# Kernel tuning notes

Measured on AMD Instinct MI355X. Metric: run time of the kernel, lower is better.

Reference implementation:

```python
import jax, jax.numpy as jnp
import numpy as np

B, P, N, E, IN, HID, NL, MULT = 4, 8, 2000, 2000, 16, 128, 3, 4
LOGIT_CLIP = 10.0

def setup_inputs() -> dict:
    key = jax.random.key(0)
    ks = jax.random.split(key, 8)
    s = 0.05
    return {
        "node_features": jax.random.normal(ks[0], (B, P, N, IN), jnp.float32),
        "incidence": jax.random.uniform(ks[1], (B, N, E), jnp.float32),  # weighted incidence
        "W_in": s * jax.random.normal(ks[2], (IN, HID), jnp.float32),
        "edge_Ws": s * jax.random.normal(ks[3], (NL, HID, HID), jnp.float32),
        "node_Ws": s * jax.random.normal(ks[4], (NL, HID, HID), jnp.float32),
        "W1": s * jax.random.normal(ks[5], (HID, MULT * HID), jnp.float32),
        "W2": s * jax.random.normal(ks[6], (MULT * HID, HID), jnp.float32),
        "W_dec": s * jax.random.normal(ks[7], (HID, 1), jnp.float32),
    }

def reference(node_features, incidence, W_in, edge_Ws, node_Ws, W1, W2, W_dec):
    # node_features: [B,P,N,in]; incidence H: [B,N,E] (broadcast over P instead of torch's repeat)
    x = node_features @ W_in                                   # [B,P,N,h]
    H = incidence
    n_layers = edge_Ws.shape[0]
    for l in range(n_layers):
        # node -> hyperedge aggregation: H^T @ x
        e = jnp.einsum('bne,bpnd->bped', H, x)                 # [B,P,E,h]
        e = jax.nn.relu(e @ edge_Ws[l])
        # hyperedge -> node aggregation: H @ e
        x = jnp.einsum('bne,bped->bpnd', H, e)                 # [B,P,N,h]
        x = jax.nn.relu(x @ node_Ws[l])
    # MLP: Linear -> ReLU -> Linear (dropout = 0)
    h = jax.nn.relu(x @ W1) @ W2                               # [B,P,N,h]
    out = h @ W_dec                                            # [B,P,N,1]
    out = out / jnp.sqrt(jnp.asarray(W_in.shape[1], jnp.float32))
    out = LOGIT_CLIP * jnp.tanh(out)
    return out
```

## Files before the change

kernel.cpp:

```cpp
#include <hip/hip_runtime.h>
#include <hip/hip_bf16.h>


typedef __attribute__((ext_vector_type(8))) short bf16x8;
typedef __attribute__((ext_vector_type(4))) float f32x4;

#define GLL16(gp, lp) __builtin_amdgcn_global_load_lds(                      \
    (const __attribute__((address_space(1))) void*)(gp),                     \
    (__attribute__((address_space(3))) void*)(lp), 16, 0, 0)

__device__ __forceinline__ unsigned short f2bf(float v) {
  __hip_bfloat16 h = __float2bfloat16(v);
  return __builtin_bit_cast(unsigned short, h);
}
__device__ __forceinline__ float bf2f(unsigned short u) {
  unsigned int x = ((unsigned int)u) << 16;
  return __builtin_bit_cast(float, x);
}

__global__ void convH_k(const float* __restrict__ H,
                        unsigned short* __restrict__ Hb,
                        unsigned short* __restrict__ HTb) {
  int b  = blockIdx.z;
  int n0 = blockIdx.y * 32, e0 = blockIdx.x * 32;
  __shared__ float t[32][33];
  int tx = threadIdx.x & 31, ty = threadIdx.x >> 5;
  for (int r = ty; r < 32; r += 8) {
    int n = n0 + r, e = e0 + tx;
    float v = (n < 2000 && e < 2000) ? H[((long)b * 2000 + n) * 2000 + e] : 0.f;
    t[r][tx] = v;
    Hb[((long)b * 2048 + n) * 2048 + e] = f2bf(v);
  }
  __syncthreads();
  for (int r = ty; r < 32; r += 8) {
    HTb[((long)b * 2048 + (e0 + r)) * 2048 + (n0 + tx)] = f2bf(t[tx][r]);
  }
}

__global__ void transposeW_k(const float* __restrict__ src,
                             unsigned short* __restrict__ dst, int R, int C) {
  __shared__ float t[32][33];
  int c0 = blockIdx.x * 32, r0 = blockIdx.y * 32;
  int tx = threadIdx.x & 31, ty = threadIdx.x >> 5;
  for (int rr = ty; rr < 32; rr += 8) {
    int rI = r0 + rr, cI = c0 + tx;
    t[rr][tx] = (rI < R && cI < C) ? src[(long)rI * C + cI] : 0.f;
  }
  __syncthreads();
  for (int rr = ty; rr < 32; rr += 8) {
    int cO = c0 + rr, rO = r0 + tx;
    if (cO < C && rO < R) dst[(long)cO * R + rO] = f2bf(t[tx][rr]);
  }
}

__global__ __launch_bounds__(256) void x0_k(
    const float* __restrict__ nf, const float* __restrict__ Win,
    unsigned short* __restrict__ xb, unsigned short* __restrict__ xTb) {
  __shared__ float nfs[128][16];
  __shared__ float wins[2048];
  __shared__ unsigned short xt[128][136];

  int bp = blockIdx.y;
  int n0 = blockIdx.x * 128;
  int tid = threadIdx.x;

  {
    int r = tid >> 1, c = (tid & 1) * 8;
    int n = n0 + r;
    float4 v0 = make_float4(0.f, 0.f, 0.f, 0.f), v1 = v0;
    if (n < 2000) {
      const float* src = nf + ((long)bp * 2000 + n) * 16 + c;
      v0 = *(const float4*)src;
      v1 = *(const float4*)(src + 4);
    }
    *(float4*)&nfs[r][c]     = v0;
    *(float4*)&nfs[r][c + 4] = v1;
  }
  {
    int base = tid * 8;
    float4 a = *(const float4*)(Win + base);
    float4 b = *(const float4*)(Win + base + 4);
    *(float4*)&wins[base]     = a;
    *(float4*)&wins[base + 4] = b;
  }
  __syncthreads();

  int d = tid & 127, half = tid >> 7;
  float wcol[16];
#pragma unroll
  for (int k = 0; k < 16; k++) wcol[k] = wins[k * 128 + d];

  unsigned short* xtRow = xTb + ((long)bp * 128 + d) * 2048 + n0 + half * 64;
#pragma unroll
  for (int oct = 0; oct < 8; oct++) {
    bf16x8 pk;
#pragma unroll
    for (int j = 0; j < 8; j++) {
      int nl = half * 64 + oct * 8 + j;
      float v = 0.f;
#pragma unroll
      for (int k = 0; k < 16; k++) v += nfs[nl][k] * wcol[k];
      unsigned short bits = f2bf(v);
      pk[j] = (short)bits;
      xt[nl][d] = bits;
    }
    *(bf16x8*)(xtRow + oct * 8) = pk;
  }
  __syncthreads();

  {
    int r = tid >> 1, c0 = (tid & 1) * 64;
    unsigned short* dst = xb + ((long)bp * 2048 + n0 + r) * 128 + c0;
#pragma unroll
    for (int i = 0; i < 8; i++) {
      bf16x8 v = *(const bf16x8*)&xt[r][c0 + i * 8];
      *(bf16x8*)(dst + i * 8) = v;
    }
  }
}

__global__ void wfuse_k(const float* __restrict__ W2, const float* __restrict__ Wdec,
                        float* __restrict__ wf) {
  int i = blockIdx.x * 256 + threadIdx.x;
  if (i < 512) {
    float s = 0.f;
#pragma unroll 8
    for (int j = 0; j < 128; j++) s += W2[i * 128 + j] * Wdec[j];
    wf[i] = s;
  }
}

template <int WN, int WT>
__global__ __launch_bounds__(256, 2) void gemm_fused(
    const unsigned short* __restrict__ A, int lda, long strideA, int aDiv,
    const unsigned short* __restrict__ BT, int ldbt, long strideBT,
    const unsigned short* __restrict__ Wt,
    unsigned short* __restrict__ Cn, int ldc, long strideCn,
    unsigned short* __restrict__ Ct, int ldct, long strideCt, int K) {
  int wgid = blockIdx.x;
  int orig = (wgid & 7) * 64 + (wgid >> 3);
  int mblk = orig & 15;
  int bz   = orig >> 4;
  A  += (long)(bz / aDiv) * strideA;
  BT += (long)bz * strideBT;
  int m0 = mblk * 128;

  __shared__ unsigned short smem[32768];

  int tid  = threadIdx.x;
  int lane = tid & 63;
  int w    = tid >> 6;
  int wr   = w >> 1, wc = w & 1;
  int fr   = lane & 15;
  int fg   = lane >> 4;

  int srow   = tid >> 3;
  int schunk = ((tid & 7) ^ (srow & 7)) * 8;
  const unsigned short* Agp[4];
  const unsigned short* Bgp[4];
#pragma unroll
  for (int i = 0; i < 4; i++) {
    Agp[i] = A + (long)(m0 + i * 32 + srow) * lda + schunk;
    Bgp[i] = BT + (long)(i * 32 + srow) * ldbt + schunk;
  }

#define STAGE(sel, tk) do {                                                  \
    long _k = (long)(tk) * 64;                                               \
    _Pragma("unroll")                                                        \
    for (int i = 0; i < 4; i++)                                              \
      GLL16(Agp[i] + _k, smem + (sel) * 16384 + (i * 256 + tid) * 8);        \
    _Pragma("unroll")                                                        \
    for (int i = 0; i < 4; i++)                                              \
      GLL16(Bgp[i] + _k, smem + (sel) * 16384 + 8192 + (i * 256 + tid) * 8); \
  } while (0)

  f32x4 acc[4][4] = {};
  const int cOff0 = (fg ^ (fr & 7)) * 8;
  const int cOff1 = ((4 + fg) ^ (fr & 7)) * 8;

#define PHASE(Asp, Bsp, CO) do {                                             \
    bf16x8 af[4], bv[4];                                                     \
    _Pragma("unroll")                                                        \
    for (int m = 0; m < 4; m++)                                              \
      af[m] = *(const bf16x8*)&(Asp)[(wr * 64 + m * 16 + fr) * 64 + (CO)];   \
    _Pragma("unroll")                                                        \
    for (int n = 0; n < 4; n++)                                              \
      bv[n] = *(const bf16x8*)&(Bsp)[(wc * 64 + n * 16 + fr) * 64 + (CO)];   \
    __builtin_amdgcn_s_setprio(1);                                           \
    _Pragma("unroll")                                                        \
    for (int m = 0; m < 4; m++)                                              \
      _Pragma("unroll")                                                      \
      for (int n = 0; n < 4; n++)                                            \
        acc[m][n] = __builtin_amdgcn_mfma_f32_16x16x32_bf16(af[m], bv[n],    \
                                                            acc[m][n], 0, 0, 0); \
    __builtin_amdgcn_s_setprio(0);                                           \
  } while (0)

#define COMPUTE64(sel) do {                                                  \
    const unsigned short* As_ = smem + (sel) * 16384;                        \
    const unsigned short* Bs_ = As_ + 8192;                                  \
    PHASE(As_, Bs_, cOff0);                                                  \
    PHASE(As_, Bs_, cOff1);                                                  \
  } while (0)

#define VMW(n) asm volatile("s_waitcnt vmcnt(" #n ")" ::: "memory")
#define BARR __builtin_amdgcn_s_barrier()
#define SCH0 __builtin_amdgcn_sched_barrier(0)

  int nt2 = K >> 6;

  STAGE(0, 0);
  int t = 0;
  for (; t + 2 < nt2; t += 2) {
    STAGE(1, t + 1);
    VMW(8); BARR; SCH0;
    COMPUTE64(0);
    BARR;
    STAGE(0, t + 2);
    VMW(8); BARR; SCH0;
    COMPUTE64(1);
    BARR;
  }
  STAGE(1, nt2 - 1);
  VMW(8); BARR; SCH0;
  COMPUTE64(0);
  BARR;
  VMW(0); BARR; SCH0;
  COMPUTE64(1);
#undef STAGE
#undef COMPUTE64
#undef PHASE

  unsigned short* Gs = smem;
#pragma unroll
  for (int m = 0; m < 4; m++) {
#pragma unroll
    for (int n = 0; n < 4; n++) {
      int rowb = wr * 64 + m * 16 + fg * 4;
      int col  = wc * 64 + n * 16 + fr;
      int ch = col >> 3, ci = col & 7;
#pragma unroll
      for (int r = 0; r < 4; r++) {
        int row = rowb + r;
        Gs[row * 128 + ((ch ^ (row & 7)) * 8) + ci] = f2bf(acc[m][n][r]);
      }
    }
  }
  __syncthreads();

  f32x4 acc2[4][4] = {};
#pragma unroll
  for (int kk = 0; kk < 4; kk++) {
    bf16x8 a2[4], b2[4];
#pragma unroll
    for (int m = 0; m < 4; m++) {
      int row = wr * 64 + m * 16 + fr;
      int c = kk * 4 + fg;
      a2[m] = *(const bf16x8*)&Gs[row * 128 + ((c ^ (fr & 7)) * 8)];
    }
#pragma unroll
    for (int n = 0; n < 4; n++) {
      int row = wc * 64 + n * 16 + fr;
      b2[n] = *(const bf16x8*)&Wt[row * 128 + (kk * 4 + fg) * 8];
    }
#pragma unroll
    for (int m = 0; m < 4; m++)
#pragma unroll
      for (int n = 0; n < 4; n++)
        acc2[m][n] = __builtin_amdgcn_mfma_f32_16x16x32_bf16(a2[m], b2[n], acc2[m][n], 0, 0, 0);
  }

  if (WN) {
#pragma unroll
    for (int m = 0; m < 4; m++) {
#pragma unroll
      for (int n = 0; n < 4; n++) {
        int rowb = m0 + wr * 64 + m * 16 + fg * 4;
        int col  = wc * 64 + n * 16 + fr;
        unsigned short* p = Cn + bz * strideCn + (long)rowb * ldc + col;
        p[0]       = f2bf(fmaxf(acc2[m][n][0], 0.f));
        p[ldc]     = f2bf(fmaxf(acc2[m][n][1], 0.f));
        p[2 * ldc] = f2bf(fmaxf(acc2[m][n][2], 0.f));
        p[3 * ldc] = f2bf(fmaxf(acc2[m][n][3], 0.f));
      }
    }
  }

  if (WT) {
    __syncthreads();
    unsigned short* GsT = smem;
#pragma unroll
    for (int m = 0; m < 4; m++) {
#pragma unroll
      for (int n = 0; n < 4; n++) {
        int rowb = wr * 64 + m * 16 + fg * 4;
        int col  = wc * 64 + n * 16 + fr;
        int chunk = rowb >> 3;
        ushort4 pk;
        pk.x = f2bf(fmaxf(acc2[m][n][0], 0.f));
        pk.y = f2bf(fmaxf(acc2[m][n][1], 0.f));
        pk.z = f2bf(fmaxf(acc2[m][n][2], 0.f));
        pk.w = f2bf(fmaxf(acc2[m][n][3], 0.f));
        *(ushort4*)&GsT[col * 128 + ((chunk ^ (col & 7)) * 8) + (rowb & 7)] = pk;
      }
    }
    __syncthreads();
    unsigned short* CtB = Ct + bz * strideCt + m0;
#pragma unroll
    for (int i = 0; i < 8; i++) {
      int s = i * 256 + tid;
      int col = s >> 4, slot = s & 15;
      int l = slot ^ (col & 7);
      bf16x8 v = *(const bf16x8*)&GsT[col * 128 + slot * 8];
      *(bf16x8*)(CtB + (long)col * ldct + l * 8) = v;
    }
  }
}

__global__ __launch_bounds__(256) void mlp_k(
    const unsigned short* __restrict__ X,
    const unsigned short* __restrict__ W1T,
    const float* __restrict__ wf,
    float* __restrict__ out) {
  __shared__ unsigned short Xs[128 * 128];
  __shared__ unsigned short Bs[128 * 128];
  __shared__ float rowacc[128];

  int tid  = threadIdx.x;
  int lane = tid & 63;
  int w    = tid >> 6, wr = w >> 1, wc = w & 1;
  int fr   = lane & 15, fg = lane >> 4;
  long m0  = (long)blockIdx.x * 128;

#pragma unroll
  for (int i = 0; i < 8; i++) {
    int s = i * 256 + tid;
    int r = s >> 4, c = (s & 15) ^ (r & 7);
    GLL16(X + (m0 + r) * 128 + c * 8, (unsigned short*)Xs + s * 8);
  }
  if (tid < 128) rowacc[tid] = 0.f;

  float rs[4][4] = {};

  for (int nb = 0; nb < 4; nb++) {
#pragma unroll
    for (int i = 0; i < 8; i++) {
      int s = i * 256 + tid;
      int r = s >> 4, c = (s & 15) ^ (r & 7);
      GLL16(W1T + (long)(nb * 128 + r) * 128 + c * 8, (unsigned short*)Bs + s * 8);
    }
    __syncthreads();

    f32x4 acc[4][4] = {};
#pragma unroll
    for (int kk = 0; kk < 4; kk++) {
      bf16x8 a2[4], b2[4];
#pragma unroll
      for (int m = 0; m < 4; m++) {
        int row = wr * 64 + m * 16 + fr;
        int c = kk * 4 + fg;
        a2[m] = *(const bf16x8*)&Xs[row * 128 + ((c ^ (row & 7)) * 8)];
      }
#pragma unroll
      for (int n = 0; n < 4; n++) {
        int row = wc * 64 + n * 16 + fr;
        int c = kk * 4 + fg;
        b2[n] = *(const bf16x8*)&Bs[row * 128 + ((c ^ (row & 7)) * 8)];
      }
#pragma unroll
      for (int m = 0; m < 4; m++)
#pragma unroll
        for (int n = 0; n < 4; n++)
          acc[m][n] = __builtin_amdgcn_mfma_f32_16x16x32_bf16(a2[m], b2[n], acc[m][n], 0, 0, 0);
    }

#pragma unroll
    for (int n = 0; n < 4; n++) {
      float wv = wf[nb * 128 + wc * 64 + n * 16 + fr];
#pragma unroll
      for (int m = 0; m < 4; m++)
#pragma unroll
        for (int r = 0; r < 4; r++)
          rs[m][r] += fmaxf(acc[m][n][r], 0.f) * wv;
    }
    __syncthreads();
  }

#pragma unroll
  for (int m = 0; m < 4; m++)
#pragma unroll
    for (int r = 0; r < 4; r++) {
      float v = rs[m][r];
      v += __shfl_xor(v, 1, 64);
      v += __shfl_xor(v, 2, 64);
      v += __shfl_xor(v, 4, 64);
      v += __shfl_xor(v, 8, 64);
      if (fr == 0) atomicAdd(&rowacc[wr * 64 + m * 16 + fg * 4 + r], v);
    }
  __syncthreads();

  if (tid < 128) {
    long row = m0 + tid;
    int bp = (int)(row >> 11), n = (int)(row & 2047);
    if (n < 2000)
      out[(long)bp * 2000 + n] = 10.f * tanhf(rowacc[tid] * 0.08838834764831843f);
  }
}

extern "C" void kernel_launch(void* const* d_in, const int* in_sizes, int n_in,
                              void* d_out, int out_size, void* d_ws, size_t ws_size,
                              hipStream_t stream) {
  const float* nf    = (const float*)d_in[0];
  const float* H     = (const float*)d_in[1];
  const float* Win   = (const float*)d_in[2];
  const float* edgeW = (const float*)d_in[3];
  const float* nodeW = (const float*)d_in[4];
  const float* W1    = (const float*)d_in[5];
  const float* W2    = (const float*)d_in[6];
  const float* Wdec  = (const float*)d_in[7];
  float* out = (float*)d_out;

  char* ws = (char*)d_ws;
  unsigned short* Hb   = (unsigned short*)(ws + 0);
  unsigned short* HTb  = (unsigned short*)(ws + 33554432);
  unsigned short* xb   = (unsigned short*)(ws + 67108864);
  unsigned short* xTb  = (unsigned short*)(ws + 83886080);
  unsigned short* eTb  = (unsigned short*)(ws + 100663296);
  unsigned short* edgeWT = (unsigned short*)(ws + 117440512);
  unsigned short* nodeWT = (unsigned short*)(ws + 117538816);
  unsigned short* W1T    = (unsigned short*)(ws + 117637120);
  float*          wf     = (float*)(ws + 117768192);
  (void)ws_size; (void)in_sizes; (void)n_in; (void)out_size;

  convH_k<<<dim3(64, 64, 4), 256, 0, stream>>>(H, Hb, HTb);
  for (int l = 0; l < 3; l++) {
    transposeW_k<<<dim3(4, 4), 256, 0, stream>>>(edgeW + l * 16384, edgeWT + l * 16384, 128, 128);
    transposeW_k<<<dim3(4, 4), 256, 0, stream>>>(nodeW + l * 16384, nodeWT + l * 16384, 128, 128);
  }
  transposeW_k<<<dim3(16, 4), 256, 0, stream>>>(W1, W1T, 128, 512);
  wfuse_k<<<2, 256, 0, stream>>>(W2, Wdec, wf);
  x0_k<<<dim3(16, 32), 256, 0, stream>>>(nf, Win, xb, xTb);

  for (int l = 0; l < 3; l++) {
    gemm_fused<0, 1><<<dim3(512), 256, 0, stream>>>(
        HTb, 2048, 2048L * 2048, 8, xTb, 2048, 128L * 2048,
        edgeWT + l * 16384,
        nullptr, 0, 0, eTb, 2048, 128L * 2048, 2048);
    if (l < 2) {
      gemm_fused<0, 1><<<dim3(512), 256, 0, stream>>>(
          Hb, 2048, 2048L * 2048, 8, eTb, 2048, 128L * 2048,
          nodeWT + l * 16384,
          nullptr, 0, 0, xTb, 2048, 128L * 2048, 2048);
    } else {
      gemm_fused<1, 1><<<dim3(512), 256, 0, stream>>>(
          Hb, 2048, 2048L * 2048, 8, eTb, 2048, 128L * 2048,
          nodeWT + l * 16384,
          xb, 128, 2048L * 128, xTb, 2048, 128L * 2048, 2048);
    }
  }

  mlp_k<<<dim3(512), 256, 0, stream>>>(xb, W1T, wf, out);
}
```

Baseline: 313.8 us.

## Replace LDS double-buffered staging with direct global loads into MFMA fragments

Removes the global_load_lds double-buffered pipeline with its barriers and swizzled LDS tiles. Each wave now loads its A and B fragments straight from global memory into registers every K-step. LDS shrinks to a single 128x128 epilogue buffer, which may raise occupancy. In exchange, reuse of the tile across waves through LDS is lost, so each wave re-reads data from global/L2, and loads are no longer overlapped with compute by an explicit prefetch.

```diff
diff --git a/kernel.cpp b/kernel.cpp
--- a/kernel.cpp
+++ b/kernel.cpp
@@ -145,7 +145,7 @@
   BT += (long)bz * strideBT;
   int m0 = mblk * 128;
 
-  __shared__ unsigned short smem[32768];
+  __shared__ unsigned short Gs[128 * 128];
 
   int tid  = threadIdx.x;
   int lane = tid & 63;
@@ -154,84 +154,41 @@
   int fr   = lane & 15;
   int fg   = lane >> 4;
 
-  int srow   = tid >> 3;
-  int schunk = ((tid & 7) ^ (srow & 7)) * 8;
-  const unsigned short* Agp[4];
-  const unsigned short* Bgp[4];
-#pragma unroll
-  for (int i = 0; i < 4; i++) {
-    Agp[i] = A + (long)(m0 + i * 32 + srow) * lda + schunk;
-    Bgp[i] = BT + (long)(i * 32 + srow) * ldbt + schunk;
-  }
-
-#define STAGE(sel, tk) do {                                                  \
-    long _k = (long)(tk) * 64;                                               \
-    _Pragma("unroll")                                                        \
-    for (int i = 0; i < 4; i++)                                              \
-      GLL16(Agp[i] + _k, smem + (sel) * 16384 + (i * 256 + tid) * 8);        \
-    _Pragma("unroll")                                                        \
-    for (int i = 0; i < 4; i++)                                              \
-      GLL16(Bgp[i] + _k, smem + (sel) * 16384 + 8192 + (i * 256 + tid) * 8); \
-  } while (0)
+  const unsigned short* Arow[4];
+  const unsigned short* Bcol[4];
+#pragma unroll
+  for (int m = 0; m < 4; m++)
+    Arow[m] = A + (long)(m0 + wr * 64 + m * 16 + fr) * lda + fg * 8;
+#pragma unroll
+  for (int n = 0; n < 4; n++)
+    Bcol[n] = BT + (long)(wc * 64 + n * 16 + fr) * ldbt + fg * 8;
 
   f32x4 acc[4][4] = {};
-  const int cOff0 = (fg ^ (fr & 7)) * 8;
-  const int cOff1 = ((4 + fg) ^ (fr & 7)) * 8;
-
-#define PHASE(Asp, Bsp, CO) do {                                             \
-    bf16x8 af[4], bv[4];                                                     \
-    _Pragma("unroll")                                                        \
-    for (int m = 0; m < 4; m++)                                              \
-      af[m] = *(const bf16x8*)&(Asp)[(wr * 64 + m * 16 + fr) * 64 + (CO)];   \
-    _Pragma("unroll")                                                        \
-    for (int n = 0; n < 4; n++)                                              \
-      bv[n] = *(const bf16x8*)&(Bsp)[(wc * 64 + n * 16 + fr) * 64 + (CO)];   \
-    __builtin_amdgcn_s_setprio(1);                                           \
-    _Pragma("unroll")                                                        \
-    for (int m = 0; m < 4; m++)                                              \
-      _Pragma("unroll")                                                      \
-      for (int n = 0; n < 4; n++)                                            \
-        acc[m][n] = __builtin_amdgcn_mfma_f32_16x16x32_bf16(af[m], bv[n],    \
-                                                            acc[m][n], 0, 0, 0); \
-    __builtin_amdgcn_s_setprio(0);                                           \
-  } while (0)
-
-#define COMPUTE64(sel) do {                                                  \
-    const unsigned short* As_ = smem + (sel) * 16384;                        \
-    const unsigned short* Bs_ = As_ + 8192;                                  \
-    PHASE(As_, Bs_, cOff0);                                                  \
-    PHASE(As_, Bs_, cOff1);                                                  \
-  } while (0)
-
-#define VMW(n) asm volatile("s_waitcnt vmcnt(" #n ")" ::: "memory")
-#define BARR __builtin_amdgcn_s_barrier()
-#define SCH0 __builtin_amdgcn_sched_barrier(0)
-
-  int nt2 = K >> 6;
-
-  STAGE(0, 0);
-  int t = 0;
-  for (; t + 2 < nt2; t += 2) {
-    STAGE(1, t + 1);
-    VMW(8); BARR; SCH0;
-    COMPUTE64(0);
-    BARR;
-    STAGE(0, t + 2);
-    VMW(8); BARR; SCH0;
-    COMPUTE64(1);
-    BARR;
-  }
-  STAGE(1, nt2 - 1);
-  VMW(8); BARR; SCH0;
-  COMPUTE64(0);
-  BARR;
-  VMW(0); BARR; SCH0;
-  COMPUTE64(1);
-#undef STAGE
-#undef COMPUTE64
-#undef PHASE
-
-  unsigned short* Gs = smem;
+
+  for (int k0 = 0; k0 < K; k0 += 64) {
+    bf16x8 a0[4], a1[4], b0[4], b1[4];
+#pragma unroll
+    for (int m = 0; m < 4; m++) {
+      a0[m] = *(const bf16x8*)(Arow[m] + k0);
+      a1[m] = *(const bf16x8*)(Arow[m] + k0 + 32);
+    }
+#pragma unroll
+    for (int n = 0; n < 4; n++) {
+      b0[n] = *(const bf16x8*)(Bcol[n] + k0);
+      b1[n] = *(const bf16x8*)(Bcol[n] + k0 + 32);
+    }
+#pragma unroll
+    for (int m = 0; m < 4; m++)
+#pragma unroll
+      for (int n = 0; n < 4; n++)
+        acc[m][n] = __builtin_amdgcn_mfma_f32_16x16x32_bf16(a0[m], b0[n], acc[m][n], 0, 0, 0);
+#pragma unroll
+    for (int m = 0; m < 4; m++)
+#pragma unroll
+      for (int n = 0; n < 4; n++)
+        acc[m][n] = __builtin_amdgcn_mfma_f32_16x16x32_bf16(a1[m], b1[n], acc[m][n], 0, 0, 0);
+  }
+
 #pragma unroll
   for (int m = 0; m < 4; m++) {
 #pragma unroll
@@ -288,7 +245,7 @@
 
   if (WT) {
     __syncthreads();
-    unsigned short* GsT = smem;
+    unsigned short* GsT = Gs;
 #pragma unroll
     for (int m = 0; m < 4; m++) {
 #pragma unroll
```

After: 816.0 us. 160% more time.

## Split K across two wave groups per block with LDS reduction in fused GEMM

Applied to the files above, without the earlier changes.

The fused hypergraph GEMM now launches 512 threads per block, split into two 256-thread groups. Each group handles half of the K dimension with its own double-buffered 32-wide K tiles in shared memory. The partial accumulators are then summed through an fp32 LDS reduction before group 0 runs the weight GEMM and the epilogue. The aim is more waves per CU to hide memory latency on a grid of only 512 blocks. In exchange it adds an LDS reduction with extra barriers, leaves half the threads idle in the epilogue, and increases register pressure under the stricter launch bounds.

```diff
diff --git a/kernel.cpp b/kernel.cpp
--- a/kernel.cpp
+++ b/kernel.cpp
@@ -131,7 +131,7 @@
 }
 
 template <int WN, int WT>
-__global__ __launch_bounds__(256, 2) void gemm_fused(
+__global__ __launch_bounds__(512, 4) void gemm_fused(
     const unsigned short* __restrict__ A, int lda, long strideA, int aDiv,
     const unsigned short* __restrict__ BT, int ldbt, long strideBT,
     const unsigned short* __restrict__ Wt,
@@ -148,44 +148,47 @@
   __shared__ unsigned short smem[32768];
 
   int tid  = threadIdx.x;
+  int grp  = tid >> 8;
+  int gtid = tid & 255;
   int lane = tid & 63;
-  int w    = tid >> 6;
-  int wr   = w >> 1, wc = w & 1;
+  int wig  = (tid >> 6) & 3;
+  int wr   = wig >> 1, wc = wig & 1;
   int fr   = lane & 15;
   int fg   = lane >> 4;
 
-  int srow   = tid >> 3;
-  int schunk = ((tid & 7) ^ (srow & 7)) * 8;
-  const unsigned short* Agp[4];
-  const unsigned short* Bgp[4];
-#pragma unroll
-  for (int i = 0; i < 4; i++) {
-    Agp[i] = A + (long)(m0 + i * 32 + srow) * lda + schunk;
-    Bgp[i] = BT + (long)(i * 32 + srow) * ldbt + schunk;
-  }
+  int kbase = grp * (K >> 1);
+  int nt = (K >> 1) >> 5;
+
+  int ch0 = gtid, ch1 = gtid + 256;
+  int r0_ = ch0 >> 2, gc0 = (ch0 & 3) ^ ((r0_ >> 1) & 3);
+  int r1_ = ch1 >> 2, gc1 = (ch1 & 3) ^ ((r1_ >> 1) & 3);
+  const unsigned short* Ag0 = A + (long)(m0 + r0_) * lda + kbase + gc0 * 8;
+  const unsigned short* Ag1 = A + (long)(m0 + r1_) * lda + kbase + gc1 * 8;
+  const unsigned short* Bg0 = BT + (long)r0_ * ldbt + kbase + gc0 * 8;
+  const unsigned short* Bg1 = BT + (long)r1_ * ldbt + kbase + gc1 * 8;
+  unsigned short* db = smem + grp * 16384;
 
 #define STAGE(sel, tk) do {                                                  \
-    long _k = (long)(tk) * 64;                                               \
-    _Pragma("unroll")                                                        \
-    for (int i = 0; i < 4; i++)                                              \
-      GLL16(Agp[i] + _k, smem + (sel) * 16384 + (i * 256 + tid) * 8);        \
-    _Pragma("unroll")                                                        \
-    for (int i = 0; i < 4; i++)                                              \
-      GLL16(Bgp[i] + _k, smem + (sel) * 16384 + 8192 + (i * 256 + tid) * 8); \
+    int _k = (tk) * 32;                                                      \
+    GLL16(Ag0 + _k, db + (sel) * 8192 + ch0 * 8);                            \
+    GLL16(Ag1 + _k, db + (sel) * 8192 + ch1 * 8);                            \
+    GLL16(Bg0 + _k, db + (sel) * 8192 + 4096 + ch0 * 8);                     \
+    GLL16(Bg1 + _k, db + (sel) * 8192 + 4096 + ch1 * 8);                     \
   } while (0)
 
   f32x4 acc[4][4] = {};
-  const int cOff0 = (fg ^ (fr & 7)) * 8;
-  const int cOff1 = ((4 + fg) ^ (fr & 7)) * 8;
-
-#define PHASE(Asp, Bsp, CO) do {                                             \
+  const int cIdx = (fg ^ ((fr >> 1) & 3)) * 8;
+
+#define COMPUTE(sel) do {                                                    \
+    const unsigned short* As_ = db + (sel) * 8192;                           \
+    const unsigned short* Bs_ = As_ + 4096;                                  \
     bf16x8 af[4], bv[4];                                                     \
     _Pragma("unroll")                                                        \
     for (int m = 0; m < 4; m++)                                              \
-      af[m] = *(const bf16x8*)&(Asp)[(wr * 64 + m * 16 + fr) * 64 + (CO)];   \
+      af[m] = *(const bf16x8*)&As_[(wr * 64 + m * 16 + fr) * 32 + cIdx];     \
     _Pragma("unroll")                                                        \
     for (int n = 0; n < 4; n++)                                              \
-      bv[n] = *(const bf16x8*)&(Bsp)[(wc * 64 + n * 16 + fr) * 64 + (CO)];   \
+      bv[n] = *(const bf16x8*)&Bs_[(wc * 64 + n * 16 + fr) * 32 + cIdx];     \
     __builtin_amdgcn_s_setprio(1);                                           \
     _Pragma("unroll")                                                        \
     for (int m = 0; m < 4; m++)                                              \
@@ -196,92 +199,113 @@
     __builtin_amdgcn_s_setprio(0);                                           \
   } while (0)
 
-#define COMPUTE64(sel) do {                                                  \
-    const unsigned short* As_ = smem + (sel) * 16384;                        \
-    const unsigned short* Bs_ = As_ + 8192;                                  \
-    PHASE(As_, Bs_, cOff0);                                                  \
-    PHASE(As_, Bs_, cOff1);                                                  \
-  } while (0)
-
 #define VMW(n) asm volatile("s_waitcnt vmcnt(" #n ")" ::: "memory")
 #define BARR __builtin_amdgcn_s_barrier()
 #define SCH0 __builtin_amdgcn_sched_barrier(0)
 
-  int nt2 = K >> 6;
-
   STAGE(0, 0);
   int t = 0;
-  for (; t + 2 < nt2; t += 2) {
+  for (; t + 2 < nt; t += 2) {
     STAGE(1, t + 1);
-    VMW(8); BARR; SCH0;
-    COMPUTE64(0);
+    VMW(4); BARR; SCH0;
+    COMPUTE(0);
     BARR;
     STAGE(0, t + 2);
-    VMW(8); BARR; SCH0;
-    COMPUTE64(1);
+    VMW(4); BARR; SCH0;
+    COMPUTE(1);
     BARR;
   }
-  STAGE(1, nt2 - 1);
-  VMW(8); BARR; SCH0;
-  COMPUTE64(0);
+  STAGE(1, nt - 1);
+  VMW(4); BARR; SCH0;
+  COMPUTE(0);
   BARR;
   VMW(0); BARR; SCH0;
-  COMPUTE64(1);
+  COMPUTE(1);
 #undef STAGE
-#undef COMPUTE64
-#undef PHASE
+#undef COMPUTE
+
+  float* Lf = (float*)smem;
+  __syncthreads();
+  if (grp == 1) {
+#pragma unroll
+    for (int m = 0; m < 4; m++)
+#pragma unroll
+      for (int n = 0; n < 4; n++) {
+        int rowb = wr * 64 + m * 16 + fg * 4;
+        int col  = wc * 64 + n * 16 + fr;
+#pragma unroll
+        for (int r = 0; r < 4; r++) Lf[(rowb + r) * 128 + col] = acc[m][n][r];
+      }
+  }
+  __syncthreads();
+  if (grp == 0) {
+#pragma unroll
+    for (int m = 0; m < 4; m++)
+#pragma unroll
+      for (int n = 0; n < 4; n++) {
+        int rowb = wr * 64 + m * 16 + fg * 4;
+        int col  = wc * 64 + n * 16 + fr;
+#pragma unroll
+        for (int r = 0; r < 4; r++) acc[m][n][r] += Lf[(rowb + r) * 128 + col];
+      }
+  }
+  __syncthreads();
 
   unsigned short* Gs = smem;
-#pragma unroll
-  for (int m = 0; m < 4; m++) {
-#pragma unroll
-    for (int n = 0; n < 4; n++) {
-      int rowb = wr * 64 + m * 16 + fg * 4;
-      int col  = wc * 64 + n * 16 + fr;
-      int ch = col >> 3, ci = col & 7;
-#pragma unroll
-      for (int r = 0; r < 4; r++) {
-        int row = rowb + r;
-        Gs[row * 128 + ((ch ^ (row & 7)) * 8) + ci] = f2bf(acc[m][n][r]);
+  if (grp == 0) {
+#pragma unroll
+    for (int m = 0; m < 4; m++) {
+#pragma unroll
+      for (int n = 0; n < 4; n++) {
+        int rowb = wr * 64 + m * 16 + fg * 4;
+        int col  = wc * 64 + n * 16 + fr;
+        int ch = col >> 3, ci = col & 7;
+#pragma unroll
+        for (int r = 0; r < 4; r++) {
+          int row = rowb + r;
+          Gs[row * 128 + ((ch ^ (row & 7)) * 8) + ci] = f2bf(acc[m][n][r]);
+        }
       }
     }
   }
   __syncthreads();
 
   f32x4 acc2[4][4] = {};
-#pragma unroll
-  for (int kk = 0; kk < 4; kk++) {
-    bf16x8 a2[4], b2[4];
-#pragma unroll
-    for (int m = 0; m < 4; m++) {
-      int row = wr * 64 + m * 16 + fr;
-      int c = kk * 4 + fg;
-      a2[m] = *(const bf16x8*)&Gs[row * 128 + ((c ^ (fr & 7)) * 8)];
-    }
-#pragma unroll
-    for (int n = 0; n < 4; n++) {
-      int row = wc * 64 + n * 16 + fr;
-      b2[n] = *(const bf16x8*)&Wt[row * 128 + (kk * 4 + fg) * 8];
-    }
-#pragma unroll
-    for (int m = 0; m < 4; m++)
-#pragma unroll
-      for (int n = 0; n < 4; n++)
-        acc2[m][n] = __builtin_amdgcn_mfma_f32_16x16x32_bf16(a2[m], b2[n], acc2[m][n], 0, 0, 0);
-  }
-
-  if (WN) {
-#pragma unroll
-    for (int m = 0; m < 4; m++) {
+  if (grp == 0) {
+#pragma unroll
+    for (int kk = 0; kk < 4; kk++) {
+      bf16x8 a2[4], b2[4];
+#pragma unroll
+      for (int m = 0; m < 4; m++) {
+        int row = wr * 64 + m * 16 + fr;
+        int c = kk * 4 + fg;
+        a2[m] = *(const bf16x8*)&Gs[row * 128 + ((c ^ (fr & 7)) * 8)];
+      }
 #pragma unroll
       for (int n = 0; n < 4; n++) {
-        int rowb = m0 + wr * 64 + m * 16 + fg * 4;
-        int col  = wc * 64 + n * 16 + fr;
-        unsigned short* p = Cn + bz * strideCn + (long)rowb * ldc + col;
-        p[0]       = f2bf(fmaxf(acc2[m][n][0], 0.f));
-        p[ldc]     = f2bf(fmaxf(acc2[m][n][1], 0.f));
-        p[2 * ldc] = f2bf(fmaxf(acc2[m][n][2], 0.f));
-        p[3 * ldc] = f2bf(fmaxf(acc2[m][n][3], 0.f));
+        int row = wc * 64 + n * 16 + fr;
+        b2[n] = *(const bf16x8*)&Wt[row * 128 + (kk * 4 + fg) * 8];
+      }
+#pragma unroll
+      for (int m = 0; m < 4; m++)
+#pragma unroll
+        for (int n = 0; n < 4; n++)
+          acc2[m][n] = __builtin_amdgcn_mfma_f32_16x16x32_bf16(a2[m], b2[n], acc2[m][n], 0, 0, 0);
+    }
+
+    if (WN) {
+#pragma unroll
+      for (int m = 0; m < 4; m++) {
+#pragma unroll
+        for (int n = 0; n < 4; n++) {
+          int rowb = m0 + wr * 64 + m * 16 + fg * 4;
+          int col  = wc * 64 + n * 16 + fr;
+          unsigned short* p = Cn + bz * strideCn + (long)rowb * ldc + col;
+          p[0]       = f2bf(fmaxf(acc2[m][n][0], 0.f));
+          p[ldc]     = f2bf(fmaxf(acc2[m][n][1], 0.f));
+          p[2 * ldc] = f2bf(fmaxf(acc2[m][n][2], 0.f));
+          p[3 * ldc] = f2bf(fmaxf(acc2[m][n][3], 0.f));
+        }
       }
     }
   }
@@ -289,30 +313,34 @@
   if (WT) {
     __syncthreads();
     unsigned short* GsT = smem;
-#pragma unroll
-    for (int m = 0; m < 4; m++) {
-#pragma unroll
-      for (int n = 0; n < 4; n++) {
-        int rowb = wr * 64 + m * 16 + fg * 4;
-        int col  = wc * 64 + n * 16 + fr;
-        int chunk = rowb >> 3;
-        ushort4 pk;
-        pk.x = f2bf(fmaxf(acc2[m][n][0], 0.f));
-        pk.y = f2bf(fmaxf(acc2[m][n][1], 0.f));
-        pk.z = f2bf(fmaxf(acc2[m][n][2], 0.f));
-        pk.w = f2bf(fmaxf(acc2[m][n][3], 0.f));
-        *(ushort4*)&GsT[col * 128 + ((chunk ^ (col & 7)) * 8) + (rowb & 7)] = pk;
+    if (grp == 0) {
+#pragma unroll
+      for (int m = 0; m < 4; m++) {
+#pragma unroll
+        for (int n = 0; n < 4; n++) {
+          int rowb = wr * 64 + m * 16 + fg * 4;
+          int col  = wc * 64 + n * 16 + fr;
+          int chunk = rowb >> 3;
+          ushort4 pk;
+          pk.x = f2bf(fmaxf(acc2[m][n][0], 0.f));
+          pk.y = f2bf(fmaxf(acc2[m][n][1], 0.f));
+          pk.z = f2bf(fmaxf(acc2[m][n][2], 0.f));
+          pk.w = f2bf(fmaxf(acc2[m][n][3], 0.f));
+          *(ushort4*)&GsT[col * 128 + ((chunk ^ (col & 7)) * 8) + (rowb & 7)] = pk;
+        }
       }
     }
     __syncthreads();
-    unsigned short* CtB = Ct + bz * strideCt + m0;
-#pragma unroll
-    for (int i = 0; i < 8; i++) {
-      int s = i * 256 + tid;
-      int col = s >> 4, slot = s & 15;
-      int l = slot ^ (col & 7);
-      bf16x8 v = *(const bf16x8*)&GsT[col * 128 + slot * 8];
-      *(bf16x8*)(CtB + (long)col * ldct + l * 8) = v;
+    if (grp == 0) {
+      unsigned short* CtB = Ct + bz * strideCt + m0;
+#pragma unroll
+      for (int i = 0; i < 8; i++) {
+        int s = i * 256 + gtid;
+        int col = s >> 4, slot = s & 15;
+        int l = slot ^ (col & 7);
+        bf16x8 v = *(const bf16x8*)&GsT[col * 128 + slot * 8];
+        *(bf16x8*)(CtB + (long)col * ldct + l * 8) = v;
+      }
     }
   }
 }
@@ -442,17 +470,17 @@
   x0_k<<<dim3(16, 32), 256, 0, stream>>>(nf, Win, xb, xTb);
 
   for (int l = 0; l < 3; l++) {
-    gemm_fused<0, 1><<<dim3(512), 256, 0, stream>>>(
+    gemm_fused<0, 1><<<dim3(512), 512, 0, stream>>>(
         HTb, 2048, 2048L * 2048, 8, xTb, 2048, 128L * 2048,
         edgeWT + l * 16384,
         nullptr, 0, 0, eTb, 2048, 128L * 2048, 2048);
     if (l < 2) {
-      gemm_fused<0, 1><<<dim3(512), 256, 0, stream>>>(
+      gemm_fused<0, 1><<<dim3(512), 512, 0, stream>>>(
           Hb, 2048, 2048L * 2048, 8, eTb, 2048, 128L * 2048,
           nodeWT + l * 16384,
           nullptr, 0, 0, xTb, 2048, 128L * 2048, 2048);
     } else {
-      gemm_fused<1, 1><<<dim3(512), 256, 0, stream>>>(
+      gemm_fused<1, 1><<<dim3(512), 512, 0, stream>>>(
           Hb, 2048, 2048L * 2048, 8, eTb, 2048, 128L * 2048,
           nodeWT + l * 16384,
           xb, 128, 2048L * 128, xTb, 2048, 128L * 2048, 2048);
```

Result: slower. 379.2 us (+20.8%).

## Enlarge GEMM tile to 256 rows with 8 waves and 4-stage K pipeline

Applied to the files above, without the earlier changes.

The fused hypergraph GEMM now uses 512-thread blocks that each cover 256 output rows, half as many blocks as before. The K-step shrinks to 32, and shared memory becomes a 4-deep ring buffer. Global-to-LDS loads for future stages are issued inside the compute body, after the fragment reads. The aim is better reuse of the B tile across more rows and more overlap of memory latency with MFMA work. In exchange there are more barriers per K, larger LDS use, one block per CU, and a changed transposed-output write pattern.

```diff
diff --git a/kernel.cpp b/kernel.cpp
--- a/kernel.cpp
+++ b/kernel.cpp
@@ -131,61 +131,57 @@
 }
 
 template <int WN, int WT>
-__global__ __launch_bounds__(256, 2) void gemm_fused(
+__global__ __launch_bounds__(512, 1) void gemm_fused(
     const unsigned short* __restrict__ A, int lda, long strideA, int aDiv,
     const unsigned short* __restrict__ BT, int ldbt, long strideBT,
     const unsigned short* __restrict__ Wt,
     unsigned short* __restrict__ Cn, int ldc, long strideCn,
     unsigned short* __restrict__ Ct, int ldct, long strideCt, int K) {
   int wgid = blockIdx.x;
-  int orig = (wgid & 7) * 64 + (wgid >> 3);
-  int mblk = orig & 15;
-  int bz   = orig >> 4;
+  int orig = (wgid & 7) * 32 + (wgid >> 3);
+  int mblk = orig & 7;
+  int bz   = orig >> 3;
   A  += (long)(bz / aDiv) * strideA;
   BT += (long)bz * strideBT;
-  int m0 = mblk * 128;
-
-  __shared__ unsigned short smem[32768];
+  int m0 = mblk * 256;
+
+  __shared__ unsigned short smem[49152];
 
   int tid  = threadIdx.x;
   int lane = tid & 63;
   int w    = tid >> 6;
-  int wr   = w >> 1, wc = w & 1;
+  int wr   = w >> 1;
+  int wc   = w & 1;
   int fr   = lane & 15;
   int fg   = lane >> 4;
 
-  int srow   = tid >> 3;
-  int schunk = ((tid & 7) ^ (srow & 7)) * 8;
-  const unsigned short* Agp[4];
-  const unsigned short* Bgp[4];
-#pragma unroll
-  for (int i = 0; i < 4; i++) {
-    Agp[i] = A + (long)(m0 + i * 32 + srow) * lda + schunk;
-    Bgp[i] = BT + (long)(i * 32 + srow) * ldbt + schunk;
-  }
+  int srow = tid >> 2;
+  int sch  = ((tid & 3) ^ ((srow >> 1) & 3)) * 8;
+  const unsigned short* Ag0 = A + (long)(m0 + srow) * lda + sch;
+  const unsigned short* Ag1 = A + (long)(m0 + 128 + srow) * lda + sch;
+  const unsigned short* Bg  = BT + (long)srow * ldbt + sch;
 
 #define STAGE(sel, tk) do {                                                  \
-    long _k = (long)(tk) * 64;                                               \
-    _Pragma("unroll")                                                        \
-    for (int i = 0; i < 4; i++)                                              \
-      GLL16(Agp[i] + _k, smem + (sel) * 16384 + (i * 256 + tid) * 8);        \
-    _Pragma("unroll")                                                        \
-    for (int i = 0; i < 4; i++)                                              \
-      GLL16(Bgp[i] + _k, smem + (sel) * 16384 + 8192 + (i * 256 + tid) * 8); \
+    int _k = (tk) * 32;                                                      \
+    GLL16(Ag0 + _k, smem + (sel) * 12288 + tid * 8);                         \
+    GLL16(Ag1 + _k, smem + (sel) * 12288 + 4096 + tid * 8);                  \
+    GLL16(Bg + _k,  smem + (sel) * 12288 + 8192 + tid * 8);                  \
   } while (0)
 
   f32x4 acc[4][4] = {};
-  const int cOff0 = (fg ^ (fr & 7)) * 8;
-  const int cOff1 = ((4 + fg) ^ (fr & 7)) * 8;
-
-#define PHASE(Asp, Bsp, CO) do {                                             \
+  const int cIdx = (fg ^ ((fr >> 1) & 3)) * 8;
+
+#define TILEBODY(sel, kst, DO) do {                                          \
+    const unsigned short* As_ = smem + (sel) * 12288;                        \
+    const unsigned short* Bs_ = As_ + 8192;                                  \
     bf16x8 af[4], bv[4];                                                     \
     _Pragma("unroll")                                                        \
     for (int m = 0; m < 4; m++)                                              \
-      af[m] = *(const bf16x8*)&(Asp)[(wr * 64 + m * 16 + fr) * 64 + (CO)];   \
+      af[m] = *(const bf16x8*)&As_[(wr * 64 + m * 16 + fr) * 32 + cIdx];     \
     _Pragma("unroll")                                                        \
     for (int n = 0; n < 4; n++)                                              \
-      bv[n] = *(const bf16x8*)&(Bsp)[(wc * 64 + n * 16 + fr) * 64 + (CO)];   \
+      bv[n] = *(const bf16x8*)&Bs_[(wc * 64 + n * 16 + fr) * 32 + cIdx];     \
+    if (DO) STAGE(((sel) + 3) & 3, kst);                                     \
     __builtin_amdgcn_s_setprio(1);                                           \
     _Pragma("unroll")                                                        \
     for (int m = 0; m < 4; m++)                                              \
@@ -196,40 +192,29 @@
     __builtin_amdgcn_s_setprio(0);                                           \
   } while (0)
 
-#define COMPUTE64(sel) do {                                                  \
-    const unsigned short* As_ = smem + (sel) * 16384;                        \
-    const unsigned short* Bs_ = As_ + 8192;                                  \
-    PHASE(As_, Bs_, cOff0);                                                  \
-    PHASE(As_, Bs_, cOff1);                                                  \
-  } while (0)
-
 #define VMW(n) asm volatile("s_waitcnt vmcnt(" #n ")" ::: "memory")
 #define BARR __builtin_amdgcn_s_barrier()
 #define SCH0 __builtin_amdgcn_sched_barrier(0)
 
-  int nt2 = K >> 6;
+  int nt = K >> 5;
 
   STAGE(0, 0);
-  int t = 0;
-  for (; t + 2 < nt2; t += 2) {
-    STAGE(1, t + 1);
-    VMW(8); BARR; SCH0;
-    COMPUTE64(0);
-    BARR;
-    STAGE(0, t + 2);
-    VMW(8); BARR; SCH0;
-    COMPUTE64(1);
-    BARR;
-  }
-  STAGE(1, nt2 - 1);
-  VMW(8); BARR; SCH0;
-  COMPUTE64(0);
-  BARR;
-  VMW(0); BARR; SCH0;
-  COMPUTE64(1);
+  STAGE(1, 1);
+  STAGE(2, 2);
+  int k = 0;
+  for (; k < nt - 4; k += 4) {
+    VMW(6); BARR; SCH0; TILEBODY(0, k + 3, 1);
+    VMW(6); BARR; SCH0; TILEBODY(1, k + 4, 1);
+    VMW(6); BARR; SCH0; TILEBODY(2, k + 5, 1);
+    VMW(6); BARR; SCH0; TILEBODY(3, k + 6, 1);
+  }
+  VMW(6); BARR; SCH0; TILEBODY(0, nt - 1, 1);
+  VMW(6); BARR; SCH0; TILEBODY(1, 0, 0);
+  VMW(3); BARR; SCH0; TILEBODY(2, 0, 0);
+  VMW(0); BARR; SCH0; TILEBODY(3, 0, 0);
 #undef STAGE
-#undef COMPUTE64
-#undef PHASE
+#undef TILEBODY
+  __syncthreads();
 
   unsigned short* Gs = smem;
 #pragma unroll
@@ -295,24 +280,24 @@
       for (int n = 0; n < 4; n++) {
         int rowb = wr * 64 + m * 16 + fg * 4;
         int col  = wc * 64 + n * 16 + fr;
-        int chunk = rowb >> 3;
+        int slot = (rowb >> 3) ^ (col & 7);
         ushort4 pk;
         pk.x = f2bf(fmaxf(acc2[m][n][0], 0.f));
         pk.y = f2bf(fmaxf(acc2[m][n][1], 0.f));
         pk.z = f2bf(fmaxf(acc2[m][n][2], 0.f));
         pk.w = f2bf(fmaxf(acc2[m][n][3], 0.f));
-        *(ushort4*)&GsT[col * 128 + ((chunk ^ (col & 7)) * 8) + (rowb & 7)] = pk;
+        *(ushort4*)&GsT[col * 256 + slot * 8 + (rowb & 7)] = pk;
       }
     }
     __syncthreads();
     unsigned short* CtB = Ct + bz * strideCt + m0;
-#pragma unroll
-    for (int i = 0; i < 8; i++) {
-      int s = i * 256 + tid;
-      int col = s >> 4, slot = s & 15;
-      int l = slot ^ (col & 7);
-      bf16x8 v = *(const bf16x8*)&GsT[col * 128 + slot * 8];
-      *(bf16x8*)(CtB + (long)col * ldct + l * 8) = v;
+    int col = tid >> 2, q = tid & 3;
+#pragma unroll
+    for (int g = 0; g < 8; g++) {
+      int c16 = q * 8 + g;
+      int slot = c16 ^ (col & 7);
+      bf16x8 v = *(const bf16x8*)&GsT[col * 256 + slot * 8];
+      *(bf16x8*)(CtB + (long)col * ldct + c16 * 8) = v;
     }
   }
 }
@@ -442,17 +427,17 @@
   x0_k<<<dim3(16, 32), 256, 0, stream>>>(nf, Win, xb, xTb);
 
   for (int l = 0; l < 3; l++) {
-    gemm_fused<0, 1><<<dim3(512), 256, 0, stream>>>(
+    gemm_fused<0, 1><<<dim3(256), 512, 0, stream>>>(
         HTb, 2048, 2048L * 2048, 8, xTb, 2048, 128L * 2048,
         edgeWT + l * 16384,
         nullptr, 0, 0, eTb, 2048, 128L * 2048, 2048);
     if (l < 2) {
-      gemm_fused<0, 1><<<dim3(512), 256, 0, stream>>>(
+      gemm_fused<0, 1><<<dim3(256), 512, 0, stream>>>(
           Hb, 2048, 2048L * 2048, 8, eTb, 2048, 128L * 2048,
           nodeWT + l * 16384,
           nullptr, 0, 0, xTb, 2048, 128L * 2048, 2048);
     } else {
-      gemm_fused<1, 1><<<dim3(512), 256, 0, stream>>>(
+      gemm_fused<1, 1><<<dim3(256), 512, 0, stream>>>(
           Hb, 2048, 2048L * 2048, 8, eTb, 2048, 128L * 2048,
           nodeWT + l * 16384,
           xb, 128, 2048L * 128, xTb, 2048, 128L * 2048, 2048);
```

Measured after the change: 356.4 us. 1.14x slower.
